# Optimization experiments

Hardware: AMD Instinct MI355X
Metric: run time of the kernel (lower is better)

Reference implementation:

```python
import jax, jax.numpy as jnp
import numpy as np

N = 100000
E = 1600000
IN, HID, OUT = 128, 128, 64


def setup_inputs() -> dict:
    key = jax.random.key(0)
    k = jax.random.split(key, 8)
    x = jax.random.normal(k[0], (N, IN), dtype=jnp.float32)
    src = jax.random.randint(k[1], (E,), 0, N)
    dst = jax.random.randint(k[2], (E,), 0, N)
    # Glorot-ish init for the per-layer fc_neigh weights + biases
    W1 = jax.random.normal(k[3], (IN, HID), dtype=jnp.float32) / np.sqrt(IN)
    b1 = jnp.zeros((HID,), dtype=jnp.float32)
    W2 = jax.random.normal(k[4], (HID, OUT), dtype=jnp.float32) / np.sqrt(HID)
    b2 = jnp.zeros((OUT,), dtype=jnp.float32)
    return {"x": x, "src": src, "dst": dst, "W1": W1, "b1": b1, "W2": W2, "b2": b2}


def _sage_gcn_layer(h, src, dst, W, b):
    # DGL SAGEConv aggregator_type='gcn':
    #   neigh = sum_{u in N(v)} h_u ; h_neigh = (neigh + h_v) / (deg(v) + 1)
    #   out = h_neigh @ W + b   (fc_self unused for 'gcn')
    msg = h[src]                                              # [E, d] gather
    agg = jax.ops.segment_sum(msg, dst, num_segments=N)       # [N, d] scatter-add
    deg = jax.ops.segment_sum(jnp.ones((E,), h.dtype), dst, num_segments=N)
    h_neigh = (agg + h) / (deg[:, None] + 1.0)
    return h_neigh @ W + b


def reference(x, src, dst, W1, b1, W2, b2):
    # Dropout in eval mode (identity), as for a deterministic correctness baseline.
    h = _sage_gcn_layer(x, src, dst, W1, b1)
    h = jax.nn.relu(h)
    h = _sage_gcn_layer(h, src, dst, W2, b2)
    return h
```

## Files before the change

kernel.cpp:

```cpp
#include <hip/hip_runtime.h>

#define NN 100000
#define EE 1600000
#define FD 128
#define NBK 391
#define BCAP 5120
#define CHUNK 4096

typedef __attribute__((ext_vector_type(8))) short bf16x8;
typedef __attribute__((ext_vector_type(4))) float f32x4;

static __device__ __forceinline__ unsigned bfpack(float lo, float hi) {
  unsigned a = __float_as_uint(lo), b = __float_as_uint(hi);
  a = (a + 0x7FFFu + ((a >> 16) & 1u)) >> 16;
  b = (b + 0x7FFFu + ((b >> 16) & 1u)) >> 16;
  return a | (b << 16);
}
static __device__ __forceinline__ ushort bfround(float x) {
  unsigned u = __float_as_uint(x);
  u = (u + 0x7FFFu + ((u >> 16) & 1u)) >> 16;
  return (ushort)u;
}
static __device__ __forceinline__ float bflo(unsigned u) {
  return __uint_as_float(u << 16);
}
static __device__ __forceinline__ float bfhi(unsigned u) {
  return __uint_as_float(u & 0xFFFF0000u);
}

__global__ __launch_bounds__(256) void pass1_wconv(const int* __restrict__ src,
                                                   const int* __restrict__ dst,
                                                   unsigned* __restrict__ gcur,
                                                   unsigned* __restrict__ arena,
                                                   const float* __restrict__ W1,
                                                   const float* __restrict__ W2,
                                                   ushort* __restrict__ Wt1g,
                                                   ushort* __restrict__ Wt2g) {
  __shared__ unsigned hist[NBK + 1];
  __shared__ unsigned scan[512];
  __shared__ unsigned gpos[NBK + 1];
  __shared__ unsigned sorted[CHUNK];
  int t = threadIdx.x;

  if (blockIdx.x >= NBK) {
    int i = (int)(blockIdx.x - NBK) * 256 + t;
    if (i < 128 * 128) {
      int k = i >> 7, c = i & 127;
      Wt1g[c * 128 + k] = bfround(W1[i]);
    } else {
      int j = i - 128 * 128;
      if (j < 128 * 64) {
        int k = j >> 6, c = j & 63;
        Wt2g[c * 128 + k] = bfround(W2[j]);
      }
    }
    return;
  }

  int base = blockIdx.x * CHUNK;
  hist[t] = 0;
  if (t + 256 <= NBK) hist[t + 256] = 0;
  __syncthreads();

  int dreg[16], sreg[16];
#pragma unroll
  for (int j = 0; j < 16; ++j) {
    int e = base + t + j * 256;
    if (e < EE) {
      dreg[j] = dst[e];
      sreg[j] = src[e];
      atomicAdd(&hist[dreg[j] >> 8], 1u);
    } else {
      dreg[j] = -1;
      sreg[j] = 0;
    }
  }
  __syncthreads();

  scan[t] = (t < NBK) ? hist[t] : 0;
  scan[t + 256] = (t + 256 < NBK) ? hist[t + 256] : 0;
  __syncthreads();
  for (int d = 1; d < 512; d <<= 1) {
    unsigned r0 = (t >= d) ? scan[t - d] : 0;
    unsigned r1 = ((t + 256) >= d) ? scan[t + 256 - d] : 0;
    __syncthreads();
    scan[t] += r0;
    scan[t + 256] += r1;
    __syncthreads();
  }
  unsigned c0 = (t < NBK) ? scan[t] - hist[t] : 0;
  unsigned c1 = (t + 256 < NBK) ? scan[t + 256] - hist[t + 256] : 0;
  __syncthreads();
  if (t < NBK) hist[t] = c0;
  if (t + 256 < NBK) hist[t + 256] = c1;
  __syncthreads();

#pragma unroll
  for (int j = 0; j < 16; ++j) {
    if (dreg[j] >= 0) {
      int b = dreg[j] >> 8;
      unsigned pos = atomicAdd(&hist[b], 1u);
      sorted[pos] = ((unsigned)(dreg[j] & 255) << 20) | (unsigned)sreg[j];
    }
  }
  __syncthreads();

  if (t < NBK) {
    unsigned lo = t ? scan[t - 1] : 0;
    unsigned cntb = scan[t] - lo;
    if (cntb) gpos[t] = atomicAdd(&gcur[t], cntb);
  }
  if (t + 256 < NBK) {
    unsigned lo = scan[t + 255];
    unsigned cntb = scan[t + 256] - lo;
    if (cntb) gpos[t + 256] = atomicAdd(&gcur[t + 256], cntb);
  }
  __syncthreads();

  int w = t >> 6, lane = t & 63;
  for (int b = w; b < NBK; b += 4) {
    unsigned lo = b ? scan[b - 1] : 0;
    unsigned cntb = scan[b] - lo;
    if (!cntb) continue;
    unsigned gp = gpos[b];
    if (gp >= BCAP) continue;
    unsigned lim = min(gp + cntb, (unsigned)BCAP) - gp;
    for (unsigned i = lane; i < lim; i += 64)
      arena[(size_t)b * BCAP + gp + i] = sorted[lo + i];
  }
}

template <int NCOLS>
static __device__ __forceinline__ void gemm_body_f32(const float* __restrict__ A,
                                                     const ushort* __restrict__ Wtg,
                                                     ushort* __restrict__ out, int bid,
                                                     int t, ushort* Wt, ushort* As) {
  constexpr int NCT = NCOLS / 16;
  int node0 = bid * 64;
  for (int idx = t; idx < NCOLS * 16; idx += 256) {
    int flat = idx * 8;
    int c = flat >> 7, k = flat & 127;
    uint4 v = *reinterpret_cast<const uint4*>(Wtg + flat);
    *reinterpret_cast<uint4*>(&Wt[c * 136 + k]) = v;
  }
  {
    int r = t >> 2, cq = (t & 3) * 32;
    int row = node0 + r;
    if (row >= NN) row = NN - 1;
    const float4* s = reinterpret_cast<const float4*>(A + (size_t)row * FD + cq);
    unsigned dv[16];
#pragma unroll
    for (int q = 0; q < 8; ++q) {
      float4 f = s[q];
      dv[q * 2 + 0] = bfpack(f.x, f.y);
      dv[q * 2 + 1] = bfpack(f.z, f.w);
    }
    uint4* d = reinterpret_cast<uint4*>(&As[r * 136 + cq]);
#pragma unroll
    for (int q = 0; q < 4; ++q)
      d[q] = make_uint4(dv[q * 4 + 0], dv[q * 4 + 1], dv[q * 4 + 2], dv[q * 4 + 3]);
  }
  __syncthreads();

  int w = t >> 6, l = t & 63;
  int lr = l & 15, lq = l >> 4;
  f32x4 acc[NCT];
#pragma unroll
  for (int ct = 0; ct < NCT; ++ct) acc[ct] = (f32x4)0.0f;
  const ushort* aBase = &As[(w * 16 + lr) * 136 + lq * 8];
  const ushort* bBase = &Wt[lr * 136 + lq * 8];
#pragma unroll
  for (int ks = 0; ks < 4; ++ks) {
    bf16x8 a = *reinterpret_cast<const bf16x8*>(aBase + ks * 32);
#pragma unroll
    for (int ct = 0; ct < NCT; ++ct) {
      bf16x8 b = *reinterpret_cast<const bf16x8*>(bBase + ct * 16 * 136 + ks * 32);
      acc[ct] = __builtin_amdgcn_mfma_f32_16x16x32_bf16(a, b, acc[ct], 0, 0, 0);
    }
  }
  int rowb = node0 + w * 16 + lq * 4;
#pragma unroll
  for (int ct = 0; ct < NCT; ++ct) {
#pragma unroll
    for (int r = 0; r < 4; ++r) {
      int row = rowb + r;
      if (row < NN) out[(size_t)row * NCOLS + ct * 16 + lr] = bfround(acc[ct][r]);
    }
  }
}

__global__ __launch_bounds__(256) void pass2_gemm1(const unsigned* __restrict__ arena,
                                                   const unsigned* __restrict__ gcur,
                                                   int* __restrict__ nbr,
                                                   int* __restrict__ cur,
                                                   const float* __restrict__ x,
                                                   const ushort* __restrict__ Wt1g,
                                                   ushort* __restrict__ y1) {
  __shared__ __align__(16) char smem[52224];
  int t = threadIdx.x;

  if (blockIdx.x >= NBK) {
    gemm_body_f32<128>(x, Wt1g, y1, (int)(blockIdx.x - NBK), t, (ushort*)smem,
                       (ushort*)(smem + 34816));
    return;
  }

  unsigned* sh = (unsigned*)smem;
  unsigned* hist = sh + 512;
  unsigned* scn = hist + 256;
  unsigned* sorted = scn + 256;
  int b = blockIdx.x;

  unsigned v0 = (t < NBK) ? gcur[t] : 0;
  unsigned v1 = (t + 256 < NBK) ? gcur[t + 256] : 0;
  sh[t] = v0;
  sh[t + 256] = v1;
  __syncthreads();
  for (int d = 1; d < 512; d <<= 1) {
    unsigned r0 = (t >= d) ? sh[t - d] : 0;
    unsigned r1 = ((t + 256) >= d) ? sh[t + 256 - d] : 0;
    __syncthreads();
    sh[t] += r0;
    sh[t + 256] += r1;
    __syncthreads();
  }
  unsigned base = b ? sh[b - 1] : 0;
  unsigned cnt = min(sh[b] - base, (unsigned)BCAP);
  const unsigned* run = arena + (size_t)b * BCAP;

  hist[t] = 0;
  __syncthreads();
  for (unsigned i = t; i < cnt; i += 256) atomicAdd(&hist[run[i] >> 20], 1u);
  __syncthreads();
  scn[t] = hist[t];
  __syncthreads();
  for (int d = 1; d < 256; d <<= 1) {
    unsigned r = (t >= d) ? scn[t - d] : 0;
    __syncthreads();
    scn[t] += r;
    __syncthreads();
  }
  unsigned excl = scn[t] - hist[t];
  __syncthreads();
  hist[t] = excl;
  __syncthreads();
  for (unsigned i = t; i < cnt; i += 256) {
    unsigned v = run[i];
    unsigned pos = atomicAdd(&hist[v >> 20], 1u);
    sorted[pos] = v & 0xFFFFFu;
  }
  __syncthreads();
  for (unsigned i = t; i < cnt; i += 256) nbr[base + i] = (int)sorted[i];
  int node = b * 256 + t;
  if (node < NN) cur[node] = (int)(base + scn[t]);
}

__global__ __launch_bounds__(256) void mfma_gemm64(const ushort* __restrict__ A,
                                                   const ushort* __restrict__ Wtg,
                                                   ushort* __restrict__ out) {
  __shared__ ushort Wt[64 * 136];
  __shared__ ushort As[64 * 136];
  int t = threadIdx.x;
  int node0 = blockIdx.x * 64;

  for (int idx = t; idx < 64 * 16; idx += 256) {
    int flat = idx * 8;
    int c = flat >> 7, k = flat & 127;
    uint4 v = *reinterpret_cast<const uint4*>(Wtg + flat);
    *reinterpret_cast<uint4*>(&Wt[c * 136 + k]) = v;
  }
  {
    int r = t >> 2, cq = (t & 3) * 32;
    int row = node0 + r;
    if (row >= NN) row = NN - 1;
    const uint4* s = reinterpret_cast<const uint4*>(A + (size_t)row * FD + cq);
    uint4* d = reinterpret_cast<uint4*>(&As[r * 136 + cq]);
    d[0] = s[0]; d[1] = s[1]; d[2] = s[2]; d[3] = s[3];
  }
  __syncthreads();

  int w = t >> 6, l = t & 63;
  int lr = l & 15, lq = l >> 4;
  f32x4 acc[4];
#pragma unroll
  for (int ct = 0; ct < 4; ++ct) acc[ct] = (f32x4)0.0f;
  const ushort* aBase = &As[(w * 16 + lr) * 136 + lq * 8];
  const ushort* bBase = &Wt[lr * 136 + lq * 8];
#pragma unroll
  for (int ks = 0; ks < 4; ++ks) {
    bf16x8 a = *reinterpret_cast<const bf16x8*>(aBase + ks * 32);
#pragma unroll
    for (int ct = 0; ct < 4; ++ct) {
      bf16x8 b = *reinterpret_cast<const bf16x8*>(bBase + ct * 16 * 136 + ks * 32);
      acc[ct] = __builtin_amdgcn_mfma_f32_16x16x32_bf16(a, b, acc[ct], 0, 0, 0);
    }
  }
  int rowb = node0 + w * 16 + lq * 4;
#pragma unroll
  for (int ct = 0; ct < 4; ++ct) {
#pragma unroll
    for (int r = 0; r < 4; ++r) {
      int row = rowb + r;
      if (row < NN) out[(size_t)row * 64 + ct * 16 + lr] = bfround(acc[ct][r]);
    }
  }
}

__global__ __launch_bounds__(256) void gather128_kernel(const unsigned* __restrict__ Y,
                                                        const int* __restrict__ cur,
                                                        const int* __restrict__ nbr,
                                                        const float* __restrict__ bias,
                                                        unsigned* __restrict__ outp) {
  int wv = (blockIdx.x * 256 + threadIdx.x) >> 6;
  int v0 = wv * 2;
  if (v0 >= NN) return;
  int v1 = v0 + 1;
  int lane = threadIdx.x & 63;
  int e0a = __builtin_amdgcn_readfirstlane(v0 ? cur[v0 - 1] : 0);
  int e1a = __builtin_amdgcn_readfirstlane(cur[v0]);
  int e1b = __builtin_amdgcn_readfirstlane(cur[v1]);
  int e0b = e1a;
  float invA = 1.0f / (float)(e1a - e0a + 1);
  float invB = 1.0f / (float)(e1b - e0b + 1);

  float ax0 = 0.f, ay0 = 0.f, ax1 = 0.f, ay1 = 0.f;
  int ja = e0a, jb = e0b;
  while (ja + 4 <= e1a && jb + 4 <= e1b) {
    unsigned a0 = Y[(size_t)nbr[ja + 0] * 64 + lane];
    unsigned a1 = Y[(size_t)nbr[ja + 1] * 64 + lane];
    unsigned a2 = Y[(size_t)nbr[ja + 2] * 64 + lane];
    unsigned a3 = Y[(size_t)nbr[ja + 3] * 64 + lane];
    unsigned b0 = Y[(size_t)nbr[jb + 0] * 64 + lane];
    unsigned b1 = Y[(size_t)nbr[jb + 1] * 64 + lane];
    unsigned b2 = Y[(size_t)nbr[jb + 2] * 64 + lane];
    unsigned b3 = Y[(size_t)nbr[jb + 3] * 64 + lane];
    ax0 += (bflo(a0) + bflo(a1)) + (bflo(a2) + bflo(a3));
    ay0 += (bfhi(a0) + bfhi(a1)) + (bfhi(a2) + bfhi(a3));
    ax1 += (bflo(b0) + bflo(b1)) + (bflo(b2) + bflo(b3));
    ay1 += (bfhi(b0) + bfhi(b1)) + (bfhi(b2) + bfhi(b3));
    ja += 4;
    jb += 4;
  }
  for (; ja + 4 <= e1a; ja += 4) {
    unsigned a0 = Y[(size_t)nbr[ja + 0] * 64 + lane];
    unsigned a1 = Y[(size_t)nbr[ja + 1] * 64 + lane];
    unsigned a2 = Y[(size_t)nbr[ja + 2] * 64 + lane];
    unsigned a3 = Y[(size_t)nbr[ja + 3] * 64 + lane];
    ax0 += (bflo(a0) + bflo(a1)) + (bflo(a2) + bflo(a3));
    ay0 += (bfhi(a0) + bfhi(a1)) + (bfhi(a2) + bfhi(a3));
  }
  for (; jb + 4 <= e1b; jb += 4) {
    unsigned b0 = Y[(size_t)nbr[jb + 0] * 64 + lane];
    unsigned b1 = Y[(size_t)nbr[jb + 1] * 64 + lane];
    unsigned b2 = Y[(size_t)nbr[jb + 2] * 64 + lane];
    unsigned b3 = Y[(size_t)nbr[jb + 3] * 64 + lane];
    ax1 += (bflo(b0) + bflo(b1)) + (bflo(b2) + bflo(b3));
    ay1 += (bfhi(b0) + bfhi(b1)) + (bfhi(b2) + bfhi(b3));
  }
  for (; ja < e1a; ++ja) {
    unsigned a = Y[(size_t)nbr[ja] * 64 + lane];
    ax0 += bflo(a);
    ay0 += bfhi(a);
  }
  for (; jb < e1b; ++jb) {
    unsigned b = Y[(size_t)nbr[jb] * 64 + lane];
    ax1 += bflo(b);
    ay1 += bfhi(b);
  }
  unsigned sv0 = Y[(size_t)v0 * 64 + lane];
  unsigned sv1 = Y[(size_t)v1 * 64 + lane];
  float2 bv = reinterpret_cast<const float2*>(bias)[lane];
  float rx0 = fmaxf((ax0 + bflo(sv0)) * invA + bv.x, 0.f);
  float ry0 = fmaxf((ay0 + bfhi(sv0)) * invA + bv.y, 0.f);
  float rx1 = fmaxf((ax1 + bflo(sv1)) * invB + bv.x, 0.f);
  float ry1 = fmaxf((ay1 + bfhi(sv1)) * invB + bv.y, 0.f);
  outp[(size_t)v0 * 64 + lane] = bfpack(rx0, ry0);
  outp[(size_t)v1 * 64 + lane] = bfpack(rx1, ry1);
}

__global__ __launch_bounds__(256) void gather64_kernel(const ushort* __restrict__ Y,
                                                       const int* __restrict__ cur,
                                                       const int* __restrict__ nbr,
                                                       const float* __restrict__ bias,
                                                       float* __restrict__ out) {
  int wv = (blockIdx.x * 256 + threadIdx.x) >> 6;
  int v0 = wv * 2;
  if (v0 >= NN) return;
  int v1 = v0 + 1;
  int lane = threadIdx.x & 63;
  int e0a = __builtin_amdgcn_readfirstlane(v0 ? cur[v0 - 1] : 0);
  int e1a = __builtin_amdgcn_readfirstlane(cur[v0]);
  int e1b = __builtin_amdgcn_readfirstlane(cur[v1]);
  int e0b = e1a;
  float invA = 1.0f / (float)(e1a - e0a + 1);
  float invB = 1.0f / (float)(e1b - e0b + 1);

  float s0 = 0.f, s1 = 0.f;
  int ja = e0a, jb = e0b;
  while (ja + 4 <= e1a && jb + 4 <= e1b) {
    float a0 = __uint_as_float((unsigned)Y[(size_t)nbr[ja + 0] * 64 + lane] << 16);
    float a1 = __uint_as_float((unsigned)Y[(size_t)nbr[ja + 1] * 64 + lane] << 16);
    float a2 = __uint_as_float((unsigned)Y[(size_t)nbr[ja + 2] * 64 + lane] << 16);
    float a3 = __uint_as_float((unsigned)Y[(size_t)nbr[ja + 3] * 64 + lane] << 16);
    float b0 = __uint_as_float((unsigned)Y[(size_t)nbr[jb + 0] * 64 + lane] << 16);
    float b1 = __uint_as_float((unsigned)Y[(size_t)nbr[jb + 1] * 64 + lane] << 16);
    float b2 = __uint_as_float((unsigned)Y[(size_t)nbr[jb + 2] * 64 + lane] << 16);
    float b3 = __uint_as_float((unsigned)Y[(size_t)nbr[jb + 3] * 64 + lane] << 16);
    s0 += (a0 + a1) + (a2 + a3);
    s1 += (b0 + b1) + (b2 + b3);
    ja += 4;
    jb += 4;
  }
  for (; ja + 4 <= e1a; ja += 4) {
    float a0 = __uint_as_float((unsigned)Y[(size_t)nbr[ja + 0] * 64 + lane] << 16);
    float a1 = __uint_as_float((unsigned)Y[(size_t)nbr[ja + 1] * 64 + lane] << 16);
    float a2 = __uint_as_float((unsigned)Y[(size_t)nbr[ja + 2] * 64 + lane] << 16);
    float a3 = __uint_as_float((unsigned)Y[(size_t)nbr[ja + 3] * 64 + lane] << 16);
    s0 += (a0 + a1) + (a2 + a3);
  }
  for (; jb + 4 <= e1b; jb += 4) {
    float b0 = __uint_as_float((unsigned)Y[(size_t)nbr[jb + 0] * 64 + lane] << 16);
    float b1 = __uint_as_float((unsigned)Y[(size_t)nbr[jb + 1] * 64 + lane] << 16);
    float b2 = __uint_as_float((unsigned)Y[(size_t)nbr[jb + 2] * 64 + lane] << 16);
    float b3 = __uint_as_float((unsigned)Y[(size_t)nbr[jb + 3] * 64 + lane] << 16);
    s1 += (b0 + b1) + (b2 + b3);
  }
  for (; ja < e1a; ++ja)
    s0 += __uint_as_float((unsigned)Y[(size_t)nbr[ja] * 64 + lane] << 16);
  for (; jb < e1b; ++jb)
    s1 += __uint_as_float((unsigned)Y[(size_t)nbr[jb] * 64 + lane] << 16);

  float self0 = __uint_as_float((unsigned)Y[(size_t)v0 * 64 + lane] << 16);
  float self1 = __uint_as_float((unsigned)Y[(size_t)v1 * 64 + lane] << 16);
  float bvv = bias[lane];
  out[(size_t)v0 * 64 + lane] = (s0 + self0) * invA + bvv;
  out[(size_t)v1 * 64 + lane] = (s1 + self1) * invB + bvv;
}

extern "C" void kernel_launch(void* const* d_in, const int* in_sizes, int n_in,
                              void* d_out, int out_size, void* d_ws, size_t ws_size,
                              hipStream_t stream) {
  const float* x  = (const float*)d_in[0];
  const int* src  = (const int*)d_in[1];
  const int* dst  = (const int*)d_in[2];
  const float* W1 = (const float*)d_in[3];
  const float* b1 = (const float*)d_in[4];
  const float* W2 = (const float*)d_in[5];
  const float* b2 = (const float*)d_in[6];
  float* out = (float*)d_out;

  char* ws = (char*)d_ws;
  ushort*   Wt1g  = (ushort*)(ws + 0);
  ushort*   Wt2g  = (ushort*)(ws + 32768);
  unsigned* gcur  = (unsigned*)(ws + 49152);
  int*      cur   = (int*)(ws + 53248);
  int*      nbr   = (int*)(ws + 453248);
  unsigned* arena = (unsigned*)(ws + 6853248);
  ushort*   y1    = (ushort*)(ws + 14860928);
  ushort*   h1    = (ushort*)(ws + 40460928);
  ushort*   y2    = (ushort*)(ws + 66060928);

  const int gemmBlocks = (NN + 63) / 64;
  const int gathBlocks = (NN / 2 + 3) / 4;

  hipMemsetAsync(gcur, 0, NBK * sizeof(unsigned), stream);
  pass1_wconv<<<NBK + 96, 256, 0, stream>>>(src, dst, gcur, arena, W1, W2, Wt1g, Wt2g);
  pass2_gemm1<<<NBK + gemmBlocks, 256, 0, stream>>>(arena, gcur, nbr, cur, x, Wt1g, y1);
  gather128_kernel<<<gathBlocks, 256, 0, stream>>>((const unsigned*)y1, cur, nbr, b1,
                                                   (unsigned*)h1);
  mfma_gemm64<<<gemmBlocks, 256, 0, stream>>>(h1, Wt2g, y2);
  gather64_kernel<<<gathBlocks, 256, 0, stream>>>(y2, cur, nbr, b2, out);
}
```

Before: 184.9 us.

## Slice gather kernels by feature and spread edges across lane groups

Both neighbor-aggregation kernels now give each wave one node and one 16-byte feature slice (8 slices for the 128-wide layer, 4 for the 64-wide). The 8 lane groups of 8 lanes each handle different edges in parallel and are combined with xor shuffles at the end. The goal is more memory-level parallelism and less per-wave serialization on high-degree nodes. In exchange, every slice block rereads the CSR neighbor list, each gather is only a 32-byte segment per edge, and many more blocks are launched. Nontemporal loads and stores are also added for the index and output streams.

After: 569.3 us. 3.08x slower.

```diff
diff --git a/kernel.cpp b/kernel.cpp
--- a/kernel.cpp
+++ b/kernel.cpp
@@ -306,135 +306,118 @@
   }
 }
 
-__global__ __launch_bounds__(256) void gather128_kernel(const unsigned* __restrict__ Y,
+__global__ __launch_bounds__(256) void gather128_sliced(const unsigned* __restrict__ Y,
                                                         const int* __restrict__ cur,
                                                         const int* __restrict__ nbr,
                                                         const float* __restrict__ bias,
                                                         unsigned* __restrict__ outp) {
-  int wv = (blockIdx.x * 256 + threadIdx.x) >> 6;
-  int v0 = wv * 2;
-  if (v0 >= NN) return;
-  int v1 = v0 + 1;
+  int slice = blockIdx.x & 7;
+  int node = (blockIdx.x >> 3) * 4 + (threadIdx.x >> 6);
+  if (node >= NN) return;
   int lane = threadIdx.x & 63;
-  int e0a = __builtin_amdgcn_readfirstlane(v0 ? cur[v0 - 1] : 0);
-  int e1a = __builtin_amdgcn_readfirstlane(cur[v0]);
-  int e1b = __builtin_amdgcn_readfirstlane(cur[v1]);
-  int e0b = e1a;
-  float invA = 1.0f / (float)(e1a - e0a + 1);
-  float invB = 1.0f / (float)(e1b - e0b + 1);
-
-  float ax0 = 0.f, ay0 = 0.f, ax1 = 0.f, ay1 = 0.f;
-  int ja = e0a, jb = e0b;
-  while (ja + 4 <= e1a && jb + 4 <= e1b) {
-    unsigned a0 = Y[(size_t)nbr[ja + 0] * 64 + lane];
-    unsigned a1 = Y[(size_t)nbr[ja + 1] * 64 + lane];
-    unsigned a2 = Y[(size_t)nbr[ja + 2] * 64 + lane];
-    unsigned a3 = Y[(size_t)nbr[ja + 3] * 64 + lane];
-    unsigned b0 = Y[(size_t)nbr[jb + 0] * 64 + lane];
-    unsigned b1 = Y[(size_t)nbr[jb + 1] * 64 + lane];
-    unsigned b2 = Y[(size_t)nbr[jb + 2] * 64 + lane];
-    unsigned b3 = Y[(size_t)nbr[jb + 3] * 64 + lane];
-    ax0 += (bflo(a0) + bflo(a1)) + (bflo(a2) + bflo(a3));
-    ay0 += (bfhi(a0) + bfhi(a1)) + (bfhi(a2) + bfhi(a3));
-    ax1 += (bflo(b0) + bflo(b1)) + (bflo(b2) + bflo(b3));
-    ay1 += (bfhi(b0) + bfhi(b1)) + (bfhi(b2) + bfhi(b3));
-    ja += 4;
-    jb += 4;
-  }
-  for (; ja + 4 <= e1a; ja += 4) {
-    unsigned a0 = Y[(size_t)nbr[ja + 0] * 64 + lane];
-    unsigned a1 = Y[(size_t)nbr[ja + 1] * 64 + lane];
-    unsigned a2 = Y[(size_t)nbr[ja + 2] * 64 + lane];
-    unsigned a3 = Y[(size_t)nbr[ja + 3] * 64 + lane];
-    ax0 += (bflo(a0) + bflo(a1)) + (bflo(a2) + bflo(a3));
-    ay0 += (bfhi(a0) + bfhi(a1)) + (bfhi(a2) + bfhi(a3));
-  }
-  for (; jb + 4 <= e1b; jb += 4) {
-    unsigned b0 = Y[(size_t)nbr[jb + 0] * 64 + lane];
-    unsigned b1 = Y[(size_t)nbr[jb + 1] * 64 + lane];
-    unsigned b2 = Y[(size_t)nbr[jb + 2] * 64 + lane];
-    unsigned b3 = Y[(size_t)nbr[jb + 3] * 64 + lane];
-    ax1 += (bflo(b0) + bflo(b1)) + (bflo(b2) + bflo(b3));
-    ay1 += (bfhi(b0) + bfhi(b1)) + (bfhi(b2) + bfhi(b3));
-  }
-  for (; ja < e1a; ++ja) {
-    unsigned a = Y[(size_t)nbr[ja] * 64 + lane];
-    ax0 += bflo(a);
-    ay0 += bfhi(a);
-  }
-  for (; jb < e1b; ++jb) {
-    unsigned b = Y[(size_t)nbr[jb] * 64 + lane];
-    ax1 += bflo(b);
-    ay1 += bfhi(b);
-  }
-  unsigned sv0 = Y[(size_t)v0 * 64 + lane];
-  unsigned sv1 = Y[(size_t)v1 * 64 + lane];
-  float2 bv = reinterpret_cast<const float2*>(bias)[lane];
-  float rx0 = fmaxf((ax0 + bflo(sv0)) * invA + bv.x, 0.f);
-  float ry0 = fmaxf((ay0 + bfhi(sv0)) * invA + bv.y, 0.f);
-  float rx1 = fmaxf((ax1 + bflo(sv1)) * invB + bv.x, 0.f);
-  float ry1 = fmaxf((ay1 + bfhi(sv1)) * invB + bv.y, 0.f);
-  outp[(size_t)v0 * 64 + lane] = bfpack(rx0, ry0);
-  outp[(size_t)v1 * 64 + lane] = bfpack(rx1, ry1);
-}
-
-__global__ __launch_bounds__(256) void gather64_kernel(const ushort* __restrict__ Y,
+  int eg = lane >> 3;
+  int sl = lane & 7;
+  int base = slice * 8 + sl;
+
+  int s0 = __builtin_amdgcn_readfirstlane(node ? cur[node - 1] : 0);
+  int s1 = __builtin_amdgcn_readfirstlane(cur[node]);
+  float inv = 1.0f / (float)(s1 - s0 + 1);
+
+  float ax = 0.f, ay = 0.f;
+  int j = s0;
+  for (; j + 16 <= s1; j += 16) {
+    int n0 = __builtin_nontemporal_load(nbr + j + eg);
+    int n1 = __builtin_nontemporal_load(nbr + j + 8 + eg);
+    unsigned v0 = Y[(size_t)n0 * 64 + base];
+    unsigned v1 = Y[(size_t)n1 * 64 + base];
+    ax += bflo(v0) + bflo(v1);
+    ay += bfhi(v0) + bfhi(v1);
+  }
+  for (; j + 8 <= s1; j += 8) {
+    int n0 = __builtin_nontemporal_load(nbr + j + eg);
+    unsigned v0 = Y[(size_t)n0 * 64 + base];
+    ax += bflo(v0);
+    ay += bfhi(v0);
+  }
+  int rem = s1 - j;
+  if (eg < rem) {
+    int n0 = __builtin_nontemporal_load(nbr + j + eg);
+    unsigned v0 = Y[(size_t)n0 * 64 + base];
+    ax += bflo(v0);
+    ay += bfhi(v0);
+  }
+  ax += __shfl_xor(ax, 8);
+  ay += __shfl_xor(ay, 8);
+  ax += __shfl_xor(ax, 16);
+  ay += __shfl_xor(ay, 16);
+  ax += __shfl_xor(ax, 32);
+  ay += __shfl_xor(ay, 32);
+
+  if (eg == 0) {
+    unsigned sv = Y[(size_t)node * 64 + base];
+    float2 bv = reinterpret_cast<const float2*>(bias)[base];
+    float rx = fmaxf((ax + bflo(sv)) * inv + bv.x, 0.f);
+    float ry = fmaxf((ay + bfhi(sv)) * inv + bv.y, 0.f);
+    __builtin_nontemporal_store(bfpack(rx, ry), outp + (size_t)node * 64 + base);
+  }
+}
+
+__global__ __launch_bounds__(256) void gather64_sliced(const unsigned* __restrict__ Y,
                                                        const int* __restrict__ cur,
                                                        const int* __restrict__ nbr,
                                                        const float* __restrict__ bias,
                                                        float* __restrict__ out) {
-  int wv = (blockIdx.x * 256 + threadIdx.x) >> 6;
-  int v0 = wv * 2;
-  if (v0 >= NN) return;
-  int v1 = v0 + 1;
+  int slice = blockIdx.x & 3;
+  int node = (blockIdx.x >> 2) * 4 + (threadIdx.x >> 6);
+  if (node >= NN) return;
   int lane = threadIdx.x & 63;
-  int e0a = __builtin_amdgcn_readfirstlane(v0 ? cur[v0 - 1] : 0);
-  int e1a = __builtin_amdgcn_readfirstlane(cur[v0]);
-  int e1b = __builtin_amdgcn_readfirstlane(cur[v1]);
-  int e0b = e1a;
-  float invA = 1.0f / (float)(e1a - e0a + 1);
-  float invB = 1.0f / (float)(e1b - e0b + 1);
-
-  float s0 = 0.f, s1 = 0.f;
-  int ja = e0a, jb = e0b;
-  while (ja + 4 <= e1a && jb + 4 <= e1b) {
-    float a0 = __uint_as_float((unsigned)Y[(size_t)nbr[ja + 0] * 64 + lane] << 16);
-    float a1 = __uint_as_float((unsigned)Y[(size_t)nbr[ja + 1] * 64 + lane] << 16);
-    float a2 = __uint_as_float((unsigned)Y[(size_t)nbr[ja + 2] * 64 + lane] << 16);
-    float a3 = __uint_as_float((unsigned)Y[(size_t)nbr[ja + 3] * 64 + lane] << 16);
-    float b0 = __uint_as_float((unsigned)Y[(size_t)nbr[jb + 0] * 64 + lane] << 16);
-    float b1 = __uint_as_float((unsigned)Y[(size_t)nbr[jb + 1] * 64 + lane] << 16);
-    float b2 = __uint_as_float((unsigned)Y[(size_t)nbr[jb + 2] * 64 + lane] << 16);
-    float b3 = __uint_as_float((unsigned)Y[(size_t)nbr[jb + 3] * 64 + lane] << 16);
-    s0 += (a0 + a1) + (a2 + a3);
-    s1 += (b0 + b1) + (b2 + b3);
-    ja += 4;
-    jb += 4;
-  }
-  for (; ja + 4 <= e1a; ja += 4) {
-    float a0 = __uint_as_float((unsigned)Y[(size_t)nbr[ja + 0] * 64 + lane] << 16);
-    float a1 = __uint_as_float((unsigned)Y[(size_t)nbr[ja + 1] * 64 + lane] << 16);
-    float a2 = __uint_as_float((unsigned)Y[(size_t)nbr[ja + 2] * 64 + lane] << 16);
-    float a3 = __uint_as_float((unsigned)Y[(size_t)nbr[ja + 3] * 64 + lane] << 16);
-    s0 += (a0 + a1) + (a2 + a3);
-  }
-  for (; jb + 4 <= e1b; jb += 4) {
-    float b0 = __uint_as_float((unsigned)Y[(size_t)nbr[jb + 0] * 64 + lane] << 16);
-    float b1 = __uint_as_float((unsigned)Y[(size_t)nbr[jb + 1] * 64 + lane] << 16);
-    float b2 = __uint_as_float((unsigned)Y[(size_t)nbr[jb + 2] * 64 + lane] << 16);
-    float b3 = __uint_as_float((unsigned)Y[(size_t)nbr[jb + 3] * 64 + lane] << 16);
-    s1 += (b0 + b1) + (b2 + b3);
-  }
-  for (; ja < e1a; ++ja)
-    s0 += __uint_as_float((unsigned)Y[(size_t)nbr[ja] * 64 + lane] << 16);
-  for (; jb < e1b; ++jb)
-    s1 += __uint_as_float((unsigned)Y[(size_t)nbr[jb] * 64 + lane] << 16);
-
-  float self0 = __uint_as_float((unsigned)Y[(size_t)v0 * 64 + lane] << 16);
-  float self1 = __uint_as_float((unsigned)Y[(size_t)v1 * 64 + lane] << 16);
-  float bvv = bias[lane];
-  out[(size_t)v0 * 64 + lane] = (s0 + self0) * invA + bvv;
-  out[(size_t)v1 * 64 + lane] = (s1 + self1) * invB + bvv;
+  int eg = lane >> 3;
+  int sl = lane & 7;
+  int base = slice * 8 + sl;
+
+  int s0 = __builtin_amdgcn_readfirstlane(node ? cur[node - 1] : 0);
+  int s1 = __builtin_amdgcn_readfirstlane(cur[node]);
+  float inv = 1.0f / (float)(s1 - s0 + 1);
+
+  float ax = 0.f, ay = 0.f;
+  int j = s0;
+  for (; j + 16 <= s1; j += 16) {
+    int n0 = __builtin_nontemporal_load(nbr + j + eg);
+    int n1 = __builtin_nontemporal_load(nbr + j + 8 + eg);
+    unsigned v0 = Y[(size_t)n0 * 32 + base];
+    unsigned v1 = Y[(size_t)n1 * 32 + base];
+    ax += bflo(v0) + bflo(v1);
+    ay += bfhi(v0) + bfhi(v1);
+  }
+  for (; j + 8 <= s1; j += 8) {
+    int n0 = __builtin_nontemporal_load(nbr + j + eg);
+    unsigned v0 = Y[(size_t)n0 * 32 + base];
+    ax += bflo(v0);
+    ay += bfhi(v0);
+  }
+  int rem = s1 - j;
+  if (eg < rem) {
+    int n0 = __builtin_nontemporal_load(nbr + j + eg);
+    unsigned v0 = Y[(size_t)n0 * 32 + base];
+    ax += bflo(v0);
+    ay += bfhi(v0);
+  }
+  ax += __shfl_xor(ax, 8);
+  ay += __shfl_xor(ay, 8);
+  ax += __shfl_xor(ax, 16);
+  ay += __shfl_xor(ay, 16);
+  ax += __shfl_xor(ax, 32);
+  ay += __shfl_xor(ay, 32);
+
+  if (eg == 0) {
+    unsigned sv = Y[(size_t)node * 32 + base];
+    float2 bv = reinterpret_cast<const float2*>(bias)[base];
+    union { float2 f; unsigned long long u; } cvt;
+    cvt.f.x = (ax + bflo(sv)) * inv + bv.x;
+    cvt.f.y = (ay + bfhi(sv)) * inv + bv.y;
+    __builtin_nontemporal_store(
+        cvt.u, reinterpret_cast<unsigned long long*>(out + (size_t)node * 64 + base * 2));
+  }
 }
 
 extern "C" void kernel_launch(void* const* d_in, const int* in_sizes, int n_in,
@@ -461,13 +444,14 @@
   ushort*   y2    = (ushort*)(ws + 66060928);
 
   const int gemmBlocks = (NN + 63) / 64;
-  const int gathBlocks = (NN / 2 + 3) / 4;
+  const int g128Blocks = (NN / 4) * 8;
+  const int g64Blocks  = (NN / 4) * 4;
 
   hipMemsetAsync(gcur, 0, NBK * sizeof(unsigned), stream);
   pass1_wconv<<<NBK + 96, 256, 0, stream>>>(src, dst, gcur, arena, W1, W2, Wt1g, Wt2g);
   pass2_gemm1<<<NBK + gemmBlocks, 256, 0, stream>>>(arena, gcur, nbr, cur, x, Wt1g, y1);
-  gather128_kernel<<<gathBlocks, 256, 0, stream>>>((const unsigned*)y1, cur, nbr, b1,
+  gather128_sliced<<<g128Blocks, 256, 0, stream>>>((const unsigned*)y1, cur, nbr, b1,
                                                    (unsigned*)h1);
   mfma_gemm64<<<gemmBlocks, 256, 0, stream>>>(h1, Wt2g, y2);
-  gather64_kernel<<<gathBlocks, 256, 0, stream>>>(y2, cur, nbr, b2, out);
-}
+  gather64_sliced<<<g64Blocks, 256, 0, stream>>>((const unsigned*)y2, cur, nbr, b2, out);
+}
```
